# Optimization experiments

Hardware: AMD Instinct MI355X
Metric: run time of the kernel (lower is better)

The kernel has to match this reference:

```python
import jax, jax.numpy as jnp
import numpy as np


def setup_inputs() -> dict:
    key = jax.random.key(0)
    kq, kk, kv = jax.random.split(key, 3)
    B, L, S, H, E = 2, 2048, 2048, 8, 64
    queries = jax.random.normal(kq, (B, L, H, E), dtype=jnp.float32)
    keys = jax.random.normal(kk, (B, S, H, E), dtype=jnp.float32)
    values = jax.random.normal(kv, (B, S, H, E), dtype=jnp.float32)
    a1 = jnp.float32(1.0)
    a2 = jnp.float32(1.0)
    return {"queries": queries, "keys": keys, "values": values, "a1": a1, "a2": a2}


def reference(queries, keys, values, a1, a2):
    # queries: (B,L,H,E); keys/values: (B,S,H,E)
    E = queries.shape[-1]
    scale = 1.0 / jnp.sqrt(jnp.float32(E))
    # shared QK scores: (B,H,L,S)
    qk = jnp.einsum('blhe,bshe->bhls', queries, keys) * scale
    # sparse branch: relu^2 (dropout = identity in eval)
    ssa = jnp.square(jax.nn.relu(qk))
    ssa_out = jnp.einsum('bhls,bshd->blhd', ssa, values)
    # dense branch: softmax over keys
    dsa = jax.nn.softmax(qk, axis=-1)
    dsa_out = jnp.einsum('bhls,bshd->blhd', dsa, values)
    w1 = jnp.exp(a1)
    w2 = jnp.exp(a2)
    alpha1 = w1 / (w1 + w2)
    alpha2 = w2 / (w1 + w2)
    return alpha1 * ssa_out + alpha2 * dsa_out
```

## Files before the change

### kernel.cpp

```cpp
#include <hip/hip_runtime.h>

typedef short short4v __attribute__((ext_vector_type(4)));
typedef short short8v __attribute__((ext_vector_type(8)));
typedef float float4v __attribute__((ext_vector_type(4)));
typedef unsigned short u16;

#define NB 2
#define NL 2048
#define NS 2048
#define NH 8
#define NE 64
#define HE (NH*NE)
#define NLT (NL/64)
#define NST (NS/64)

static __device__ __forceinline__ unsigned pk2bf(float a, float b) {
  union { float f; unsigned u; } x, y; x.f = a; y.f = b;
  return __builtin_amdgcn_perm(y.u + 0x8000u, x.u + 0x8000u, 0x07060302u);
}

__global__ __launch_bounds__(256, 2)
void assa_fwd(const float* __restrict__ qp, const float* __restrict__ kp,
              const float* __restrict__ vp, const float* __restrict__ a1p,
              const float* __restrict__ a2p, float* __restrict__ op)
{
  __shared__ u16 lds_k[64*64];
  __shared__ u16 lds_vt[64*64];

  const int tid  = threadIdx.x;
  const int wv   = tid >> 6;
  const int lane = tid & 63;
  const int ln15 = lane & 15;
  const int ln7  = lane & 7;
  const int quad = lane >> 4;

  const int bid = blockIdx.x;
  const int bh  = bid & 15;
  const int lt  = bid >> 4;
  const int h   = bh & (NH - 1);
  const int b   = bh >> 3;

  const int lbase = lt * 64 + wv * 16;

  short8v qf0, qf1;
  {
    const float* qrow = qp + ((size_t)(b * NL + lbase + ln15)) * HE + h * NE + quad * 8;
    float4 q0 = *(const float4*)(qrow);
    float4 q1 = *(const float4*)(qrow + 4);
    float4 q2 = *(const float4*)(qrow + 32);
    float4 q3 = *(const float4*)(qrow + 36);
    unsigned d0[4] = { pk2bf(q0.x,q0.y), pk2bf(q0.z,q0.w), pk2bf(q1.x,q1.y), pk2bf(q1.z,q1.w) };
    unsigned d1[4] = { pk2bf(q2.x,q2.y), pk2bf(q2.z,q2.w), pk2bf(q3.x,q3.y), pk2bf(q3.z,q3.w) };
    qf0 = *(const short8v*)d0;
    qf1 = *(const short8v*)d1;
  }

  const size_t kvb = (size_t)b * NS * HE + h * NE;
  const float* kb = kp + kvb;
  const float* vb = vp + kvb;

  const int rsub = lane >> 3;
  const int cg   = ln7 ^ rsub;
  const float* kpl = kb + (size_t)(wv * 16 + rsub) * HE + cg * 8;
  const float* vpl = vb + (size_t)(wv * 16) * HE + lane;

  float4 kpre[4];
  float  vpre[16];

  kpre[0] = *(const float4*)(kpl);
  kpre[1] = *(const float4*)(kpl + 4);
  kpre[2] = *(const float4*)(kpl + 8 * HE);
  kpre[3] = *(const float4*)(kpl + 8 * HE + 4);
  #pragma unroll
  for (int jj = 0; jj < 16; ++jj) vpre[jj] = vpl[(size_t)jj * HE];

  float4v acc_s[4], acc_d[4];
  #pragma unroll
  for (int t = 0; t < 4; ++t)
    #pragma unroll
    for (int r = 0; r < 4; ++r) { acc_s[t][r] = 0.0f; acc_d[t][r] = 0.0f; }

  float l_part = 0.0f;

  for (int st = 0; st < NST; ++st) {
    __syncthreads();

    #pragma unroll
    for (int i = 0; i < 2; ++i) {
      const int srow = wv * 16 + i * 8 + rsub;
      unsigned kd[4] = { pk2bf(kpre[2*i].x, kpre[2*i].y), pk2bf(kpre[2*i].z, kpre[2*i].w),
                         pk2bf(kpre[2*i+1].x, kpre[2*i+1].y), pk2bf(kpre[2*i+1].z, kpre[2*i+1].w) };
      *(int4*)(&lds_k[srow * 64 + ln7 * 8]) = *(const int4*)kd;
    }
    #pragma unroll
    for (int i = 0; i < 2; ++i) {
      const int cs = (2 * wv + i) ^ ln7;
      unsigned vd[4] = { pk2bf(vpre[8*i+0], vpre[8*i+1]), pk2bf(vpre[8*i+2], vpre[8*i+3]),
                         pk2bf(vpre[8*i+4], vpre[8*i+5]), pk2bf(vpre[8*i+6], vpre[8*i+7]) };
      *(int4*)(&lds_vt[lane * 64 + cs * 8]) = *(const int4*)vd;
    }
    __syncthreads();

    if (st + 1 < NST) {
      const float* kn = kpl + (size_t)(st + 1) * 64 * HE;
      const float* vn = vpl + (size_t)(st + 1) * 64 * HE;
      kpre[0] = *(const float4*)(kn);
      kpre[1] = *(const float4*)(kn + 4);
      kpre[2] = *(const float4*)(kn + 8 * HE);
      kpre[3] = *(const float4*)(kn + 8 * HE + 4);
      #pragma unroll
      for (int jj = 0; jj < 16; ++jj) vpre[jj] = vn[(size_t)jj * HE];
    }

    #pragma unroll
    for (int u = 0; u < 4; ++u) {
      float4v sa; sa[0] = 0.0f; sa[1] = 0.0f; sa[2] = 0.0f; sa[3] = 0.0f;
      short8v kf0 = *(const short8v*)(&lds_k[(u * 16 + ln15) * 64 + ((quad ^ ln7) * 8)]);
      short8v kf1 = *(const short8v*)(&lds_k[(u * 16 + ln15) * 64 + (((4 + quad) ^ ln7) * 8)]);
      sa = __builtin_amdgcn_mfma_f32_16x16x32_bf16(kf0, qf0, sa, 0, 0, 0);
      sa = __builtin_amdgcn_mfma_f32_16x16x32_bf16(kf1, qf1, sa, 0, 0, 0);

      float ps[4], pd[4];
      #pragma unroll
      for (int r = 0; r < 4; ++r) {
        float sc = sa[r] * 0.125f;
        float rl = sc > 0.0f ? sc : 0.0f;
        ps[r] = rl * rl;
        pd[r] = __expf(sc);
        l_part += pd[r];
      }
      unsigned da[2] = { pk2bf(ps[0], ps[1]), pk2bf(ps[2], ps[3]) };
      unsigned db[2] = { pk2bf(pd[0], pd[1]), pk2bf(pd[2], pd[3]) };
      short4v as = *(const short4v*)da;
      short4v ad = *(const short4v*)db;
      #pragma unroll
      for (int t = 0; t < 4; ++t) {
        short4v vf = *(const short4v*)(&lds_vt[(t * 16 + ln15) * 64 +
                        (((2 * u + (quad >> 1)) ^ ln7) * 8) + (quad & 1) * 4]);
        acc_s[t] = __builtin_amdgcn_mfma_f32_16x16x16bf16_1k(as, vf, acc_s[t], 0, 0, 0);
        acc_d[t] = __builtin_amdgcn_mfma_f32_16x16x16bf16_1k(ad, vf, acc_d[t], 0, 0, 0);
      }
    }
  }

  l_part += __shfl_xor(l_part, 16, 64);
  l_part += __shfl_xor(l_part, 32, 64);

  const float a1v = a1p[0];
  const float a2v = a2p[0];
  const float w1 = __expf(a1v), w2 = __expf(a2v);
  const float al1 = w1 / (w1 + w2);
  const float al2 = w2 / (w1 + w2);

  float c_d[4];
  #pragma unroll
  for (int r = 0; r < 4; ++r) {
    float ls = __shfl(l_part, quad * 4 + r, 64);
    c_d[r] = al2 / ls;
  }

  #pragma unroll
  for (int t = 0; t < 4; ++t) {
    #pragma unroll
    for (int r = 0; r < 4; ++r) {
      float val = al1 * acc_s[t][r] + c_d[r] * acc_d[t][r];
      const int l = lbase + quad * 4 + r;
      const int e = t * 16 + ln15;
      op[((size_t)(b * NL + l)) * HE + h * NE + e] = val;
    }
  }
}

extern "C" void kernel_launch(void* const* d_in, const int* in_sizes, int n_in,
                              void* d_out, int out_size, void* d_ws, size_t ws_size,
                              hipStream_t stream) {
  const float* q  = (const float*)d_in[0];
  const float* k  = (const float*)d_in[1];
  const float* v  = (const float*)d_in[2];
  const float* a1 = (const float*)d_in[3];
  const float* a2 = (const float*)d_in[4];
  float* out = (float*)d_out;
  (void)in_sizes; (void)n_in; (void)out_size; (void)d_ws; (void)ws_size;
  dim3 grid(NB * NH * NLT);
  assa_fwd<<<grid, dim3(256), 0, stream>>>(q, k, v, a1, a2, out);
}
```

Measured before the change: 131.1 us.

## Prepack K/V to swizzled bf16 tiles and stream them via global_load_lds double buffer

```diff
diff --git a/kernel.cpp b/kernel.cpp
--- a/kernel.cpp
+++ b/kernel.cpp
@@ -13,19 +13,57 @@
 #define HE (NH*NE)
 #define NLT (NL/64)
 #define NST (NS/64)
+#define TILE_U16 4096
 
 static __device__ __forceinline__ unsigned pk2bf(float a, float b) {
   union { float f; unsigned u; } x, y; x.f = a; y.f = b;
   return __builtin_amdgcn_perm(y.u + 0x8000u, x.u + 0x8000u, 0x07060302u);
 }
 
+#define GLD16(gp, lp) __builtin_amdgcn_global_load_lds( \
+    (const __attribute__((address_space(1))) void*)(gp), \
+    (__attribute__((address_space(3))) void*)(lp), 16, 0, 0)
+
+__global__ __launch_bounds__(256)
+void prepack(const float* __restrict__ kp, const float* __restrict__ vp,
+             u16* __restrict__ kimg, u16* __restrict__ vimg)
+{
+  const int tile = blockIdx.x;
+  const int st = tile & (NST - 1);
+  const int bh = tile >> 5;
+  const int h  = bh & (NH - 1);
+  const int b  = bh >> 3;
+  const int s0 = st * 64;
+  const size_t base = (size_t)b * NS * HE + h * NE;
+
+  u16* kt = kimg + (size_t)tile * TILE_U16;
+  u16* vt = vimg + (size_t)tile * TILE_U16;
+
+  for (int slot = threadIdx.x; slot < 512; slot += 256) {
+    const int srow = slot >> 3, p = slot & 7, c = p ^ (srow & 7);
+    const float* src = kp + base + (size_t)(s0 + srow) * HE + c * 8;
+    float4 x0 = *(const float4*)src;
+    float4 x1 = *(const float4*)(src + 4);
+    unsigned d[4] = { pk2bf(x0.x, x0.y), pk2bf(x0.z, x0.w),
+                      pk2bf(x1.x, x1.y), pk2bf(x1.z, x1.w) };
+    *(int4*)(kt + slot * 8) = *(const int4*)d;
+  }
+  for (int slot = threadIdx.x; slot < 512; slot += 256) {
+    const int e = slot >> 3, p = slot & 7, sc = p ^ (e & 7);
+    const float* src = vp + base + (size_t)(s0 + sc * 8) * HE + e;
+    float v0 = src[0 * HE], v1 = src[1 * HE], v2 = src[2 * HE], v3 = src[3 * HE];
+    float v4 = src[4 * HE], v5 = src[5 * HE], v6 = src[6 * HE], v7 = src[7 * HE];
+    unsigned d[4] = { pk2bf(v0, v1), pk2bf(v2, v3), pk2bf(v4, v5), pk2bf(v6, v7) };
+    *(int4*)(vt + slot * 8) = *(const int4*)d;
+  }
+}
+
 __global__ __launch_bounds__(256, 2)
-void assa_fwd(const float* __restrict__ qp, const float* __restrict__ kp,
-              const float* __restrict__ vp, const float* __restrict__ a1p,
+void assa_fwd(const float* __restrict__ qp, const u16* __restrict__ kimg,
+              const u16* __restrict__ vimg, const float* __restrict__ a1p,
               const float* __restrict__ a2p, float* __restrict__ op)
 {
-  __shared__ u16 lds_k[64*64];
-  __shared__ u16 lds_vt[64*64];
+  __shared__ __align__(16) u16 ldsb[2][2 * TILE_U16];
 
   const int tid  = threadIdx.x;
   const int wv   = tid >> 6;
@@ -49,30 +87,15 @@
     float4 q1 = *(const float4*)(qrow + 4);
     float4 q2 = *(const float4*)(qrow + 32);
     float4 q3 = *(const float4*)(qrow + 36);
-    unsigned d0[4] = { pk2bf(q0.x,q0.y), pk2bf(q0.z,q0.w), pk2bf(q1.x,q1.y), pk2bf(q1.z,q1.w) };
-    unsigned d1[4] = { pk2bf(q2.x,q2.y), pk2bf(q2.z,q2.w), pk2bf(q3.x,q3.y), pk2bf(q3.z,q3.w) };
+    unsigned d0[4] = { pk2bf(0.125f*q0.x, 0.125f*q0.y), pk2bf(0.125f*q0.z, 0.125f*q0.w),
+                       pk2bf(0.125f*q1.x, 0.125f*q1.y), pk2bf(0.125f*q1.z, 0.125f*q1.w) };
+    unsigned d1[4] = { pk2bf(0.125f*q2.x, 0.125f*q2.y), pk2bf(0.125f*q2.z, 0.125f*q2.w),
+                       pk2bf(0.125f*q3.x, 0.125f*q3.y), pk2bf(0.125f*q3.z, 0.125f*q3.w) };
     qf0 = *(const short8v*)d0;
     qf1 = *(const short8v*)d1;
   }
 
-  const size_t kvb = (size_t)b * NS * HE + h * NE;
-  const float* kb = kp + kvb;
-  const float* vb = vp + kvb;
-
-  const int rsub = lane >> 3;
-  const int cg   = ln7 ^ rsub;
-  const float* kpl = kb + (size_t)(wv * 16 + rsub) * HE + cg * 8;
-  const float* vpl = vb + (size_t)(wv * 16) * HE + lane;
-
-  float4 kpre[4];
-  float  vpre[16];
-
-  kpre[0] = *(const float4*)(kpl);
-  kpre[1] = *(const float4*)(kpl + 4);
-  kpre[2] = *(const float4*)(kpl + 8 * HE);
-  kpre[3] = *(const float4*)(kpl + 8 * HE + 4);
-  #pragma unroll
-  for (int jj = 0; jj < 16; ++jj) vpre[jj] = vpl[(size_t)jj * HE];
+  const size_t tbase = (size_t)bh * NST;
 
   float4v acc_s[4], acc_d[4];
   #pragma unroll
@@ -82,48 +105,45 @@
 
   float l_part = 0.0f;
 
+  auto dma_tile = [&](int st, int nb) {
+    const int half = wv & 1;
+    const u16* g;
+    u16* l;
+    if (wv < 2) {
+      g = kimg + (tbase + st) * TILE_U16 + half * 2048 + lane * 8;
+      l = &ldsb[nb][half * 2048];
+    } else {
+      g = vimg + (tbase + st) * TILE_U16 + half * 2048 + lane * 8;
+      l = &ldsb[nb][TILE_U16 + half * 2048];
+    }
+    GLD16(g,        l);
+    GLD16(g +  512, l +  512);
+    GLD16(g + 1024, l + 1024);
+    GLD16(g + 1536, l + 1536);
+  };
+
+  dma_tile(0, 0);
+
   for (int st = 0; st < NST; ++st) {
+    __builtin_amdgcn_s_waitcnt(0);
     __syncthreads();
-
-    #pragma unroll
-    for (int i = 0; i < 2; ++i) {
-      const int srow = wv * 16 + i * 8 + rsub;
-      unsigned kd[4] = { pk2bf(kpre[2*i].x, kpre[2*i].y), pk2bf(kpre[2*i].z, kpre[2*i].w),
-                         pk2bf(kpre[2*i+1].x, kpre[2*i+1].y), pk2bf(kpre[2*i+1].z, kpre[2*i+1].w) };
-      *(int4*)(&lds_k[srow * 64 + ln7 * 8]) = *(const int4*)kd;
-    }
-    #pragma unroll
-    for (int i = 0; i < 2; ++i) {
-      const int cs = (2 * wv + i) ^ ln7;
-      unsigned vd[4] = { pk2bf(vpre[8*i+0], vpre[8*i+1]), pk2bf(vpre[8*i+2], vpre[8*i+3]),
-                         pk2bf(vpre[8*i+4], vpre[8*i+5]), pk2bf(vpre[8*i+6], vpre[8*i+7]) };
-      *(int4*)(&lds_vt[lane * 64 + cs * 8]) = *(const int4*)vd;
-    }
-    __syncthreads();
-
-    if (st + 1 < NST) {
-      const float* kn = kpl + (size_t)(st + 1) * 64 * HE;
-      const float* vn = vpl + (size_t)(st + 1) * 64 * HE;
-      kpre[0] = *(const float4*)(kn);
-      kpre[1] = *(const float4*)(kn + 4);
-      kpre[2] = *(const float4*)(kn + 8 * HE);
-      kpre[3] = *(const float4*)(kn + 8 * HE + 4);
-      #pragma unroll
-      for (int jj = 0; jj < 16; ++jj) vpre[jj] = vn[(size_t)jj * HE];
-    }
+    if (st + 1 < NST) dma_tile(st + 1, (st + 1) & 1);
+
+    const u16* kb_l = ldsb[st & 1];
+    const u16* vb_l = ldsb[st & 1] + TILE_U16;
 
     #pragma unroll
     for (int u = 0; u < 4; ++u) {
       float4v sa; sa[0] = 0.0f; sa[1] = 0.0f; sa[2] = 0.0f; sa[3] = 0.0f;
-      short8v kf0 = *(const short8v*)(&lds_k[(u * 16 + ln15) * 64 + ((quad ^ ln7) * 8)]);
-      short8v kf1 = *(const short8v*)(&lds_k[(u * 16 + ln15) * 64 + (((4 + quad) ^ ln7) * 8)]);
+      short8v kf0 = *(const short8v*)(&kb_l[(u * 16 + ln15) * 64 + ((quad ^ ln7) * 8)]);
+      short8v kf1 = *(const short8v*)(&kb_l[(u * 16 + ln15) * 64 + (((4 + quad) ^ ln7) * 8)]);
       sa = __builtin_amdgcn_mfma_f32_16x16x32_bf16(kf0, qf0, sa, 0, 0, 0);
       sa = __builtin_amdgcn_mfma_f32_16x16x32_bf16(kf1, qf1, sa, 0, 0, 0);
 
       float ps[4], pd[4];
       #pragma unroll
       for (int r = 0; r < 4; ++r) {
-        float sc = sa[r] * 0.125f;
+        float sc = sa[r];
         float rl = sc > 0.0f ? sc : 0.0f;
         ps[r] = rl * rl;
         pd[r] = __expf(sc);
@@ -135,7 +155,7 @@
       short4v ad = *(const short4v*)db;
       #pragma unroll
       for (int t = 0; t < 4; ++t) {
-        short4v vf = *(const short4v*)(&lds_vt[(t * 16 + ln15) * 64 +
+        short4v vf = *(const short4v*)(&vb_l[(t * 16 + ln15) * 64 +
                         (((2 * u + (quad >> 1)) ^ ln7) * 8) + (quad & 1) * 4]);
         acc_s[t] = __builtin_amdgcn_mfma_f32_16x16x16bf16_1k(as, vf, acc_s[t], 0, 0, 0);
         acc_d[t] = __builtin_amdgcn_mfma_f32_16x16x16bf16_1k(ad, vf, acc_d[t], 0, 0, 0);
@@ -146,9 +166,7 @@
   l_part += __shfl_xor(l_part, 16, 64);
   l_part += __shfl_xor(l_part, 32, 64);
 
-  const float a1v = a1p[0];
-  const float a2v = a2p[0];
-  const float w1 = __expf(a1v), w2 = __expf(a2v);
+  const float w1 = __expf(a1p[0]), w2 = __expf(a2p[0]);
   const float al1 = w1 / (w1 + w2);
   const float al2 = w2 / (w1 + w2);
 
@@ -180,7 +198,11 @@
   const float* a1 = (const float*)d_in[3];
   const float* a2 = (const float*)d_in[4];
   float* out = (float*)d_out;
-  (void)in_sizes; (void)n_in; (void)out_size; (void)d_ws; (void)ws_size;
-  dim3 grid(NB * NH * NLT);
-  assa_fwd<<<grid, dim3(256), 0, stream>>>(q, k, v, a1, a2, out);
-}
+  (void)in_sizes; (void)n_in; (void)out_size; (void)ws_size;
+
+  u16* kimg = (u16*)d_ws;
+  u16* vimg = kimg + (size_t)NB * NH * NST * TILE_U16;
+
+  prepack<<<dim3(NB * NH * NST), dim3(256), 0, stream>>>(k, v, kimg, vimg);
+  assa_fwd<<<dim3(NB * NH * NLT), dim3(256), 0, stream>>>(q, kimg, vimg, a1, a2, out);
+}
```

After: 120.5 us. 8.0% less time.
